# Optimization experiments

Hardware: AMD Instinct MI355X
Metric: run time of the kernel (lower is better)

The kernel has to match this reference:

```python
import jax, jax.numpy as jnp
import numpy as np

B, T, NF, D, H = 4, 32, 256, 512, 8
DK = D // H


def setup_inputs() -> dict:
    key = jax.random.key(0)
    ks = jax.random.split(key, 10)
    x = jax.random.normal(ks[0], (B, T, NF, D), dtype=jnp.float32)
    adj = jax.random.randint(ks[1], (NF, NF), 0, 2, dtype=jnp.int32)
    adj = adj.at[jnp.arange(NF), jnp.arange(NF)].set(1)  # self-loops avoid all-masked rows
    s = 1.0 / np.sqrt(D)
    Wq = jax.random.normal(ks[2], (D, D), dtype=jnp.float32) * s
    Wk = jax.random.normal(ks[3], (D, D), dtype=jnp.float32) * s
    Wv = jax.random.normal(ks[4], (D, D), dtype=jnp.float32) * s
    Wo = jax.random.normal(ks[5], (D, D), dtype=jnp.float32) * s
    bq = jnp.zeros((D,), jnp.float32)
    bk = jnp.zeros((D,), jnp.float32)
    bv = jnp.zeros((D,), jnp.float32)
    bo = jnp.zeros((D,), jnp.float32)
    return {"x": x, "adj": adj, "Wq": Wq, "bq": bq, "Wk": Wk, "bk": bk,
            "Wv": Wv, "bv": bv, "Wo": Wo, "bo": bo}


def reference(x, adj, Wq, bq, Wk, bk, Wv, bv, Wo, bo):
    b, t, nf, d = x.shape
    q = x @ Wq.T + bq
    k = x @ Wk.T + bk
    v = x @ Wv.T + bv
    # split heads: [B,T,Nf,H,dk]
    qh = q.reshape(b, t, nf, H, DK)
    kh = k.reshape(b, t, nf, H, DK)
    vh = v.reshape(b, t, nf, H, DK)
    scores = jnp.einsum('btihd,btjhd->bthij', qh, kh) / jnp.sqrt(jnp.float32(DK))
    mask = (adj > 0)  # [Nf,Nf], broadcast over b,t,h
    scores = jnp.where(mask[None, None, None], scores, jnp.float32(-jnp.inf))
    attn = jax.nn.softmax(scores, axis=-1)  # dropout is identity in eval
    out = jnp.einsum('bthij,btjhd->btihd', attn, vh).reshape(b, t, nf, d)
    return out @ Wo.T + bo
```

## Files before the change

kernel.cpp:

```cpp
#include <hip/hip_runtime.h>

#define NF 256
#define H_ 8
#define M_ 32768

typedef _Float16 f16;
typedef _Float16 f16x8 __attribute__((ext_vector_type(8)));
typedef float f32x4 __attribute__((ext_vector_type(4)));
typedef unsigned short u16x8 __attribute__((ext_vector_type(8)));
typedef unsigned int u32x2 __attribute__((ext_vector_type(2)));
typedef unsigned int u32x4 __attribute__((ext_vector_type(4)));

#define GLOAD16(src, dst) \
  __builtin_amdgcn_global_load_lds((const __attribute__((address_space(1))) void*)(src), \
                                   (__attribute__((address_space(3))) void*)(dst), 16, 0, 0)

#define LDS_FENCE() do { asm volatile("s_waitcnt lgkmcnt(0)" ::: "memory"); \
                         __builtin_amdgcn_sched_barrier(0); } while (0)
#define SBAR() asm volatile("s_barrier" ::: "memory")


__device__ __forceinline__ void stageHT(const f16* __restrict__ g, int r0, int k0,
                                        f16* ldst, int wave, int lane) {
    const int key = lane >> 3;
    const int colsw = k0 + (((lane & 7) ^ key) << 3);
#pragma unroll
    for (int i = 0; i < 2; ++i) {
        int r = i * 64 + wave * 8 + key;
        GLOAD16(g + (size_t)(r0 + r) * 512 + colsw, ldst + (i * 64 + wave * 8) * 64);
    }
}

__device__ __forceinline__ void gemm256_core(const f16* __restrict__ A, const f16* __restrict__ W,
                                             int m0, int n0, f16* lds,
                                             f32x4 (&acc)[8][4], int wave, int lane) {
    const int wr = wave & 1, wc = wave >> 1;
    const int l15 = lane & 15, l4 = lane >> 4;
    stageHT(W, n0,        0, lds + 16384, wave, lane);
    stageHT(W, n0 + 128,  0, lds + 24576, wave, lane);
    stageHT(A, m0,        0, lds,         wave, lane);
    stageHT(A, m0 + 128,  0, lds + 8192,  wave, lane);
    stageHT(W, n0,       64, lds + 32768 + 16384, wave, lane);
    stageHT(W, n0 + 128, 64, lds + 32768 + 24576, wave, lane);
    asm volatile("s_waitcnt vmcnt(4)" ::: "memory");
    SBAR();
#pragma unroll
    for (int t = 0; t < 8; ++t) {
        f16* bufA = lds + (t & 1) * 32768;
        f16* bufB = bufA + 16384;
        f16* nA   = lds + ((t & 1) ^ 1) * 32768;
        f16x8 bfr[4][2];
#pragma unroll
        for (int j = 0; j < 4; ++j)
#pragma unroll
            for (int kk = 0; kk < 2; ++kk) {
                int rb = wc * 64 + j * 16 + l15;
                bfr[j][kk] = *reinterpret_cast<const f16x8*>(
                    bufB + rb * 64 + ((((kk << 2) + l4) ^ (rb & 7)) << 3));
            }
#pragma unroll
        for (int q = 0; q < 4; ++q) {
            f16x8 afr[2][2];
#pragma unroll
            for (int rf = 0; rf < 2; ++rf)
#pragma unroll
                for (int kk = 0; kk < 2; ++kk) {
                    int ra = wr * 128 + q * 32 + rf * 16 + l15;
                    afr[rf][kk] = *reinterpret_cast<const f16x8*>(
                        bufA + ra * 64 + ((((kk << 2) + l4) ^ (ra & 7)) << 3));
                }
            if (q == 0 && t < 7) stageHT(A, m0,       (t + 1) * 64, nA,          wave, lane);
            if (q == 1 && t < 7) stageHT(A, m0 + 128, (t + 1) * 64, nA + 8192,   wave, lane);
            if (q == 2 && t < 6) stageHT(W, n0,       (t + 2) * 64, bufB,        wave, lane);
            if (q == 3 && t < 6) stageHT(W, n0 + 128, (t + 2) * 64, bufB + 8192, wave, lane);
            SBAR();
            LDS_FENCE();
            __builtin_amdgcn_s_setprio(1);
#pragma unroll
            for (int rf = 0; rf < 2; ++rf)
#pragma unroll
                for (int j = 0; j < 4; ++j)
#pragma unroll
                    for (int kk = 0; kk < 2; ++kk)
                        acc[q * 2 + rf][j] = __builtin_amdgcn_mfma_f32_16x16x32_f16(
                            afr[rf][kk], bfr[j][kk], acc[q * 2 + rf][j], 0, 0, 0);
            __builtin_amdgcn_s_setprio(0);
            if (q < 3) SBAR();
        }
        if (t < 6) { asm volatile("s_waitcnt vmcnt(4)" ::: "memory"); }
        else       { asm volatile("s_waitcnt vmcnt(0)" ::: "memory"); }
        SBAR();
    }
}


#define QSCALE 0.1803368801111204f

__global__ void prep_all(const float* __restrict__ x, f16* __restrict__ xh,
                         const float* __restrict__ Wq, const float* __restrict__ Wk,
                         const float* __restrict__ Wv, const float* __restrict__ Wo,
                         const float* __restrict__ bq, const float* __restrict__ bk,
                         const float* __restrict__ bv, const int* __restrict__ adj,
                         f16* __restrict__ Wh, f16* __restrict__ Woh,
                         float* __restrict__ biasAll, unsigned long long* __restrict__ bmask) {
    if (blockIdx.x < 2048) {
        int idx = blockIdx.x * 256 + threadIdx.x;
        for (; idx < M_ * 512 / 8; idx += 2048 * 256) {
            const float4* s = reinterpret_cast<const float4*>(x + (size_t)idx * 8);
            float4 v0 = s[0], v1 = s[1];
            f16x8 o;
            o[0] = (f16)v0.x; o[1] = (f16)v0.y; o[2] = (f16)v0.z; o[3] = (f16)v0.w;
            o[4] = (f16)v1.x; o[5] = (f16)v1.y; o[6] = (f16)v1.z; o[7] = (f16)v1.w;
            *reinterpret_cast<f16x8*>(xh + (size_t)idx * 8) = o;
        }
        return;
    }
    const int tid = (blockIdx.x - 2048) * 256 + threadIdx.x;
    {
        const float* s; f16* d; float sc = 1.0f;
        int pp = tid >> 15, off = tid & 32767;
        if (pp == 0)      { s = Wq; d = Wh;              sc = QSCALE; }
        else if (pp == 1) { s = Wk; d = Wh + 512 * 512; }
        else if (pp == 2) { s = Wv; d = Wh + 2 * 512 * 512; }
        else              { s = Wo; d = Woh; }
        const float4* sv4 = reinterpret_cast<const float4*>(s + (size_t)off * 8);
        float4 v0 = sv4[0], v1 = sv4[1];
        f16x8 o;
        o[0] = (f16)(v0.x * sc); o[1] = (f16)(v0.y * sc);
        o[2] = (f16)(v0.z * sc); o[3] = (f16)(v0.w * sc);
        o[4] = (f16)(v1.x * sc); o[5] = (f16)(v1.y * sc);
        o[6] = (f16)(v1.z * sc); o[7] = (f16)(v1.w * sc);
        *reinterpret_cast<f16x8*>(d + (size_t)off * 8) = o;
    }
    if (tid < 1536) {
        float v = (tid < 512) ? QSCALE * bq[tid] : (tid < 1024) ? bk[tid - 512] : bv[tid - 1024];
        biasAll[tid] = v;
    }
    if (tid < 65536) {
        unsigned long long bal = __ballot(adj[tid] > 0);
        if ((tid & 63) == 0) bmask[tid >> 6] = bal;
    }
}


__global__ __launch_bounds__(512) void qkv_gemm(const f16* __restrict__ A, const f16* __restrict__ W,
                                                const float* __restrict__ biasAll,
                                                f16* __restrict__ out, f16* __restrict__ vT) {
    __shared__ __align__(16) f16 lds[65536];
    const int tt = threadIdx.x, wave = tt >> 6, lane = tt & 63;
    const int lb = blockIdx.x, xcd = lb & 7, idx = lb >> 3;
    const int m0 = (xcd * 16 + idx / 6) * 256;
    const int n0 = (idx % 6) * 256;
    f32x4 acc[8][4] = {};
    gemm256_core(A, W, m0, n0, lds, acc, wave, lane);

    const int wr = wave & 1, wc = wave >> 1;
    const int l15 = lane & 15, l4 = lane >> 4;
    f16* epi = lds;
    const bool isV = (n0 >= 1024);
    float bb[4];
#pragma unroll
    for (int bc = 0; bc < 4; ++bc) bb[bc] = biasAll[n0 + wc * 64 + bc * 16 + l15];
#pragma unroll
    for (int half = 0; half < 2; ++half) {
        if (wr == half) {
            if (!isV) {
#pragma unroll
                for (int ar = 0; ar < 8; ++ar)
#pragma unroll
                    for (int bc = 0; bc < 4; ++bc)
#pragma unroll
                        for (int r = 0; r < 4; ++r)
                            epi[(ar * 16 + l4 * 4 + r) * 264 + wc * 64 + bc * 16 + l15] =
                                (f16)(acc[ar][bc][r] + bb[bc]);
            } else {
#pragma unroll
                for (int ar = 0; ar < 8; ++ar)
#pragma unroll
                    for (int bc = 0; bc < 4; ++bc)
#pragma unroll
                        for (int r = 0; r < 4; ++r)
                            epi[(wc * 64 + bc * 16 + l15) * 136 + ar * 16 + l4 * 4 + r] =
                                (f16)(acc[ar][bc][r] + bb[bc]);
            }
        }
        LDS_FENCE();
        SBAR();
        if (!isV) {
            const int rr = tt >> 5, slot = tt & 31;
#pragma unroll
            for (int p = 0; p < 8; ++p) {
                int row = p * 16 + rr;
                *reinterpret_cast<f16x8*>(out + (size_t)(m0 + half * 128 + row) * 1024 + n0 + slot * 8) =
                    *reinterpret_cast<const f16x8*>(epi + row * 264 + slot * 8);
            }
        } else {
            f16* vdst = vT + (size_t)(m0 >> 8) * 8 * 64 * 256 + (size_t)(n0 - 1024) * 256;
            const int dk = tt >> 1;
#pragma unroll
            for (int i = 0; i < 8; ++i) {
                int nf0 = (tt & 1) * 64 + i * 8;
                *reinterpret_cast<f16x8*>(vdst + (size_t)dk * 256 + half * 128 + nf0) =
                    *reinterpret_cast<const f16x8*>(epi + dk * 136 + nf0);
            }
        }
        SBAR();
    }
}


template <int NR>
__device__ __forceinline__ void stage_rows512(const f16* __restrict__ g, int ld, int coff,
                                              f16* ldsb, int wave, int lane) {
    const int rr = wave * 8 + (lane >> 3);
    const int p  = lane & 7;
#pragma unroll
    for (int i = 0; i < NR / 64; ++i) {
        int r = i * 64 + rr;
        int col = ((p ^ (r & 7)) << 3);
        GLOAD16(g + (size_t)r * ld + coff + col, ldsb + (i * 64 + wave * 8) * 64);
    }
}

__device__ __forceinline__ void stage_v512(const f16* __restrict__ g, f16* ldsb,
                                           int wave, int lane) {
    const int rr = wave * 8 + (lane >> 3);
    const int p  = lane & 7;
#pragma unroll
    for (int i = 0; i < 4; ++i) {
        int r = i * 64 + rr;
        int key = (r ^ (r >> 3)) & 7;
        GLOAD16(g + (size_t)r * 64 + ((p ^ key) << 3), ldsb + (i * 64 + wave * 8) * 64);
    }
}

__global__ __launch_bounds__(512, 2) void attn_kernel(const f16* __restrict__ qkv,
                                                      const f16* __restrict__ vT,
                                                      const unsigned long long* __restrict__ bmg,
                                                      f16* __restrict__ ao) {
    __shared__ f16 Ks[256 * 64];
    __shared__ f16 Vs[256 * 64];
    __shared__ unsigned long long BMs[1024];
    const int t = threadIdx.x, wave = t >> 6, lane = t & 63;
    const int l15 = lane & 15, l4 = lane >> 4;
    const int lb = blockIdx.x, xcd = lb & 7, idx = lb >> 3;
    const int bt = xcd * 16 + (idx >> 3), h = idx & 7;
    const int bh = bt * 8 + h;
    const int btq = bt * 256, hq = h * 64;
    const f16* qb = qkv + (size_t)btq * 1024 + hq;
    const f16* kb = qb + 512;

    stage_rows512<256>(kb, 1024, 0, Ks, wave, lane);
    stage_v512(vT + (size_t)bh * 16384, Vs, wave, lane);
    GLOAD16((const char*)bmg + (size_t)t * 16, (char*)(BMs + wave * 128));
    __syncthreads();

    for (int s = 0; s < 2; ++s) {
        const int qrow_base = wave * 32 + s * 16;

        f16x8 aq[2];
#pragma unroll
        for (int kk = 0; kk < 2; ++kk)
            aq[kk] = *reinterpret_cast<const f16x8*>(
                qb + (size_t)(qrow_base + l15) * 1024 + kk * 32 + l4 * 8);

        f32x4 sc[16];
#pragma unroll
        for (int ct = 0; ct < 16; ++ct) sc[ct] = (f32x4){0.f, 0.f, 0.f, 0.f};
        __builtin_amdgcn_s_setprio(1);
#pragma unroll
        for (int ct = 0; ct < 16; ++ct)
#pragma unroll
            for (int kk = 0; kk < 2; ++kk) {
                int rk = ct * 16 + l15;
                int sk = kk * 4 + l4;
                f16x8 bk_ = *reinterpret_cast<const f16x8*>(Ks + rk * 64 + ((sk ^ (rk & 7)) << 3));
                sc[ct] = __builtin_amdgcn_mfma_f32_16x16x32_f16(bk_, aq[kk], sc[ct], 0, 0, 0);
            }
        __builtin_amdgcn_s_setprio(0);

        float mx = -1e38f;
#pragma unroll
        for (int ct = 0; ct < 16; ++ct)
#pragma unroll
            for (int r = 0; r < 4; ++r) mx = fmaxf(mx, sc[ct][r]);
        mx = fmaxf(mx, __shfl_xor(mx, 16, 64));
        mx = fmaxf(mx, __shfl_xor(mx, 32, 64));

        const int ig = qrow_base + l15;
        const u16x8* mr = reinterpret_cast<const u16x8*>(BMs + ig * 4);
        u16x8 w0 = mr[0], w1 = mr[1];

        f32x4 oacc[4] = {};
        float sum = 0.f;
#pragma unroll
        for (int kkp = 0; kkp < 8; ++kkp) {
            const int ctA = 2 * kkp, ctB = 2 * kkp + 1;
            unsigned mbA = ((kkp < 4) ? (unsigned)w0[ctA] : (unsigned)w1[ctA & 7]) >> (l4 * 4);
            unsigned mbB = ((kkp < 4) ? (unsigned)w0[ctB] : (unsigned)w1[ctB & 7]) >> (l4 * 4);
            float pA0 = __builtin_exp2f(sc[ctA][0] - mx); pA0 = ((mbA >> 0) & 1u) ? pA0 : 0.0f;
            float pA1 = __builtin_exp2f(sc[ctA][1] - mx); pA1 = ((mbA >> 1) & 1u) ? pA1 : 0.0f;
            float pA2 = __builtin_exp2f(sc[ctA][2] - mx); pA2 = ((mbA >> 2) & 1u) ? pA2 : 0.0f;
            float pA3 = __builtin_exp2f(sc[ctA][3] - mx); pA3 = ((mbA >> 3) & 1u) ? pA3 : 0.0f;
            float pB0 = __builtin_exp2f(sc[ctB][0] - mx); pB0 = ((mbB >> 0) & 1u) ? pB0 : 0.0f;
            float pB1 = __builtin_exp2f(sc[ctB][1] - mx); pB1 = ((mbB >> 1) & 1u) ? pB1 : 0.0f;
            float pB2 = __builtin_exp2f(sc[ctB][2] - mx); pB2 = ((mbB >> 2) & 1u) ? pB2 : 0.0f;
            float pB3 = __builtin_exp2f(sc[ctB][3] - mx); pB3 = ((mbB >> 3) & 1u) ? pB3 : 0.0f;
            sum += (pA0 + pA1) + (pA2 + pA3) + (pB0 + pB1) + (pB2 + pB3);
            u32x4 up;
            up[0] = __builtin_bit_cast(unsigned int, __builtin_amdgcn_cvt_pkrtz(pA0, pA1));
            up[1] = __builtin_bit_cast(unsigned int, __builtin_amdgcn_cvt_pkrtz(pA2, pA3));
            up[2] = __builtin_bit_cast(unsigned int, __builtin_amdgcn_cvt_pkrtz(pB0, pB1));
            up[3] = __builtin_bit_cast(unsigned int, __builtin_amdgcn_cvt_pkrtz(pB2, pB3));
            f16x8 pa = __builtin_bit_cast(f16x8, up);
            __builtin_amdgcn_s_setprio(1);
#pragma unroll
            for (int c2 = 0; c2 < 4; ++c2) {
                int d = c2 * 16 + l15;
                int nf0a = kkp * 32 + l4 * 4;
                int nf0b = nf0a + 16;
                int rvA = d * 4 + (nf0a >> 6), rvB = d * 4 + (nf0b >> 6);
                int keyA = (rvA ^ (rvA >> 3)) & 7, keyB = (rvB ^ (rvB >> 3)) & 7;
                u32x2 va = *reinterpret_cast<const u32x2*>(
                    Vs + rvA * 64 + ((((nf0a >> 3) & 7) ^ keyA) << 3) + (nf0a & 7));
                u32x2 vb = *reinterpret_cast<const u32x2*>(
                    Vs + rvB * 64 + ((((nf0b >> 3) & 7) ^ keyB) << 3) + (nf0b & 7));
                u32x4 uv; uv[0] = va[0]; uv[1] = va[1]; uv[2] = vb[0]; uv[3] = vb[1];
                f16x8 bv_ = __builtin_bit_cast(f16x8, uv);
                oacc[c2] = __builtin_amdgcn_mfma_f32_16x16x32_f16(pa, bv_, oacc[c2], 0, 0, 0);
            }
            __builtin_amdgcn_s_setprio(0);
            __builtin_amdgcn_sched_barrier(0);
        }
        sum += __shfl_xor(sum, 16, 64);
        sum += __shfl_xor(sum, 32, 64);
        float rs = 1.0f / sum;
        float rsrow[4];
#pragma unroll
        for (int r = 0; r < 4; ++r) rsrow[r] = __shfl(rs, l4 * 4 + r, 64);

#pragma unroll
        for (int c2 = 0; c2 < 4; ++c2)
#pragma unroll
            for (int r = 0; r < 4; ++r) {
                int nf = qrow_base + l4 * 4 + r;
                int dcol = hq + c2 * 16 + l15;
                ao[((size_t)btq + nf) * 512 + dcol] = (f16)(oacc[c2][r] * rsrow[r]);
            }
    }
}


__global__ __launch_bounds__(512) void o_gemm(const f16* __restrict__ A, const f16* __restrict__ W,
                                              const float* __restrict__ bo, float* __restrict__ out) {
    __shared__ __align__(16) f16 lds[65536];
    const int tt = threadIdx.x, wave = tt >> 6, lane = tt & 63;
    const int lb = blockIdx.x, xcd = lb & 7, idx = lb >> 3;
    const int m0 = (xcd * 16 + idx / 2) * 256;
    const int n0 = (idx % 2) * 256;
    f32x4 acc[8][4] = {};
    gemm256_core(A, W, m0, n0, lds, acc, wave, lane);

    const int wr = wave & 1, wc = wave >> 1;
    const int l15 = lane & 15, l4 = lane >> 4;
    float bb[4];
#pragma unroll
    for (int bc = 0; bc < 4; ++bc) bb[bc] = bo[n0 + wc * 64 + bc * 16 + l15];
#pragma unroll
    for (int ar = 0; ar < 8; ++ar)
#pragma unroll
        for (int bc = 0; bc < 4; ++bc) {
            int ng = n0 + wc * 64 + bc * 16 + l15;
#pragma unroll
            for (int r = 0; r < 4; ++r) {
                int mg = m0 + wr * 128 + ar * 16 + l4 * 4 + r;
                out[(size_t)mg * 512 + ng] = acc[ar][bc][r] + bb[bc];
            }
        }
}


extern "C" void kernel_launch(void* const* d_in, const int* in_sizes, int n_in,
                              void* d_out, int out_size, void* d_ws, size_t ws_size,
                              hipStream_t stream) {
    const float* x   = (const float*)d_in[0];
    const int*   adj = (const int*)d_in[1];
    const float* Wq  = (const float*)d_in[2];
    const float* bq  = (const float*)d_in[3];
    const float* Wk  = (const float*)d_in[4];
    const float* bk  = (const float*)d_in[5];
    const float* Wv  = (const float*)d_in[6];
    const float* bv  = (const float*)d_in[7];
    const float* Wo  = (const float*)d_in[8];
    const float* bo  = (const float*)d_in[9];
    float* out = (float*)d_out;

    char* ws = (char*)d_ws;
    f16*   Wh      = (f16*)ws;
    f16*   Woh     = (f16*)(ws + 1572864);
    float* biasAll = (float*)(ws + 2097152);
    unsigned long long* bmask = (unsigned long long*)(ws + 2103296);
    f16*   xh      = (f16*)(ws + 2111488);
    f16*   qkvb    = (f16*)(ws + 2111488 + (size_t)M_ * 512 * 2);
    f16*   vTb     = (f16*)(ws + 2111488 + (size_t)M_ * 512 * 2 + (size_t)M_ * 1024 * 2);
    f16*   aob     = xh;

    prep_all<<<2560, 256, 0, stream>>>(x, xh, Wq, Wk, Wv, Wo, bq, bk, bv, adj,
                                       Wh, Woh, biasAll, bmask);
    qkv_gemm<<<768, 512, 0, stream>>>(xh, Wh, biasAll, qkvb, vTb);
    attn_kernel<<<128 * H_, 512, 0, stream>>>(qkvb, vTb, bmask, aob);
    o_gemm<<<256, 512, 0, stream>>>(aob, Woh, bo, out);
}
```

Before: 165.0 us.

## Fuse fp32-to-fp16 conversion of x into QKV GEMM A-tile loading

Removes the separate x conversion pass from the prep kernel and has the QKV GEMM load fp32 x directly into registers, convert it with packed round-toward-zero conversion, and write the f16 tile to LDS while prefetching the next k-step. This avoids writing and rereading a 32 MB fp16 copy of x. In exchange each GEMM tile reads fp32 data (twice the bytes) across the six column tiles, and uses more registers and manual LDS writes instead of asynchronous global-to-LDS loads. The rounding mode also changes from round-to-nearest to round-toward-zero.

```diff
diff --git a/kernel.cpp b/kernel.cpp
--- a/kernel.cpp
+++ b/kernel.cpp
@@ -19,6 +19,15 @@
                          __builtin_amdgcn_sched_barrier(0); } while (0)
 #define SBAR() asm volatile("s_barrier" ::: "memory")
 
+__device__ __forceinline__ f16x8 cvt8(float4 a, float4 b) {
+    u32x4 u;
+    u[0] = __builtin_bit_cast(unsigned int, __builtin_amdgcn_cvt_pkrtz(a.x, a.y));
+    u[1] = __builtin_bit_cast(unsigned int, __builtin_amdgcn_cvt_pkrtz(a.z, a.w));
+    u[2] = __builtin_bit_cast(unsigned int, __builtin_amdgcn_cvt_pkrtz(b.x, b.y));
+    u[3] = __builtin_bit_cast(unsigned int, __builtin_amdgcn_cvt_pkrtz(b.z, b.w));
+    return __builtin_bit_cast(f16x8, u);
+}
+
 
 __device__ __forceinline__ void stageHT(const f16* __restrict__ g, int r0, int k0,
                                         f16* ldst, int wave, int lane) {
@@ -30,6 +39,7 @@
         GLOAD16(g + (size_t)(r0 + r) * 512 + colsw, ldst + (i * 64 + wave * 8) * 64);
     }
 }
+
 
 __device__ __forceinline__ void gemm256_core(const f16* __restrict__ A, const f16* __restrict__ W,
                                              int m0, int n0, f16* lds,
@@ -96,26 +106,13 @@
 
 #define QSCALE 0.1803368801111204f
 
-__global__ void prep_all(const float* __restrict__ x, f16* __restrict__ xh,
-                         const float* __restrict__ Wq, const float* __restrict__ Wk,
+__global__ void prep_all(const float* __restrict__ Wq, const float* __restrict__ Wk,
                          const float* __restrict__ Wv, const float* __restrict__ Wo,
                          const float* __restrict__ bq, const float* __restrict__ bk,
                          const float* __restrict__ bv, const int* __restrict__ adj,
                          f16* __restrict__ Wh, f16* __restrict__ Woh,
                          float* __restrict__ biasAll, unsigned long long* __restrict__ bmask) {
-    if (blockIdx.x < 2048) {
-        int idx = blockIdx.x * 256 + threadIdx.x;
-        for (; idx < M_ * 512 / 8; idx += 2048 * 256) {
-            const float4* s = reinterpret_cast<const float4*>(x + (size_t)idx * 8);
-            float4 v0 = s[0], v1 = s[1];
-            f16x8 o;
-            o[0] = (f16)v0.x; o[1] = (f16)v0.y; o[2] = (f16)v0.z; o[3] = (f16)v0.w;
-            o[4] = (f16)v1.x; o[5] = (f16)v1.y; o[6] = (f16)v1.z; o[7] = (f16)v1.w;
-            *reinterpret_cast<f16x8*>(xh + (size_t)idx * 8) = o;
-        }
-        return;
-    }
-    const int tid = (blockIdx.x - 2048) * 256 + threadIdx.x;
+    const int tid = blockIdx.x * 256 + threadIdx.x;
     {
         const float* s; f16* d; float sc = 1.0f;
         int pp = tid >> 15, off = tid & 32767;
@@ -143,7 +140,7 @@
 }
 
 
-__global__ __launch_bounds__(512) void qkv_gemm(const f16* __restrict__ A, const f16* __restrict__ W,
+__global__ __launch_bounds__(512) void qkv_gemm(const float* __restrict__ x, const f16* __restrict__ W,
                                                 const float* __restrict__ biasAll,
                                                 f16* __restrict__ out, f16* __restrict__ vT) {
     __shared__ __align__(16) f16 lds[65536];
@@ -151,11 +148,114 @@
     const int lb = blockIdx.x, xcd = lb & 7, idx = lb >> 3;
     const int m0 = (xcd * 16 + idx / 6) * 256;
     const int n0 = (idx % 6) * 256;
-    f32x4 acc[8][4] = {};
-    gemm256_core(A, W, m0, n0, lds, acc, wave, lane);
-
     const int wr = wave & 1, wc = wave >> 1;
     const int l15 = lane & 15, l4 = lane >> 4;
+    const int key = lane >> 3, p = lane & 7;
+    const int colsw = ((p ^ key) << 3);
+    f32x4 acc[8][4] = {};
+    float4 lA[8];
+
+    stageHT(W, n0,        0, lds + 16384, wave, lane);
+    stageHT(W, n0 + 128,  0, lds + 24576, wave, lane);
+#pragma unroll
+    for (int half = 0; half < 2; ++half)
+#pragma unroll
+        for (int i = 0; i < 2; ++i) {
+            const float* src = x + (size_t)(m0 + half * 128 + i * 64 + wave * 8 + key) * 512 + colsw;
+            lA[half * 4 + i * 2]     = *reinterpret_cast<const float4*>(src);
+            lA[half * 4 + i * 2 + 1] = *reinterpret_cast<const float4*>(src + 4);
+        }
+    stageHT(W, n0,       64, lds + 32768 + 16384, wave, lane);
+    stageHT(W, n0 + 128, 64, lds + 32768 + 24576, wave, lane);
+#pragma unroll
+    for (int half = 0; half < 2; ++half)
+#pragma unroll
+        for (int i = 0; i < 2; ++i)
+            *reinterpret_cast<f16x8*>(lds + half * 8192 + (i * 64 + wave * 8 + key) * 64 + p * 8) =
+                cvt8(lA[half * 4 + i * 2], lA[half * 4 + i * 2 + 1]);
+    asm volatile("s_waitcnt vmcnt(4)" ::: "memory");
+    asm volatile("s_waitcnt lgkmcnt(0)" ::: "memory");
+    SBAR();
+
+#pragma unroll
+    for (int t = 0; t < 8; ++t) {
+        f16* bufA = lds + (t & 1) * 32768;
+        f16* bufB = bufA + 16384;
+        f16* nA   = lds + ((t & 1) ^ 1) * 32768;
+        f16x8 bfr[4][2];
+#pragma unroll
+        for (int j = 0; j < 4; ++j)
+#pragma unroll
+            for (int kk = 0; kk < 2; ++kk) {
+                int rb = wc * 64 + j * 16 + l15;
+                bfr[j][kk] = *reinterpret_cast<const f16x8*>(
+                    bufB + rb * 64 + ((((kk << 2) + l4) ^ (rb & 7)) << 3));
+            }
+#pragma unroll
+        for (int q = 0; q < 4; ++q) {
+            f16x8 afr[2][2];
+#pragma unroll
+            for (int rf = 0; rf < 2; ++rf)
+#pragma unroll
+                for (int kk = 0; kk < 2; ++kk) {
+                    int ra = wr * 128 + q * 32 + rf * 16 + l15;
+                    afr[rf][kk] = *reinterpret_cast<const f16x8*>(
+                        bufA + ra * 64 + ((((kk << 2) + l4) ^ (ra & 7)) << 3));
+                }
+            if (q == 0 && t < 7) {
+#pragma unroll
+                for (int i = 0; i < 2; ++i) {
+                    const float* src = x + (size_t)(m0 + i * 64 + wave * 8 + key) * 512 + (t + 1) * 64 + colsw;
+                    lA[i * 2]     = *reinterpret_cast<const float4*>(src);
+                    lA[i * 2 + 1] = *reinterpret_cast<const float4*>(src + 4);
+                }
+            }
+            if (q == 1 && t < 7) {
+#pragma unroll
+                for (int i = 0; i < 2; ++i) {
+                    const float* src = x + (size_t)(m0 + 128 + i * 64 + wave * 8 + key) * 512 + (t + 1) * 64 + colsw;
+                    lA[4 + i * 2]     = *reinterpret_cast<const float4*>(src);
+                    lA[4 + i * 2 + 1] = *reinterpret_cast<const float4*>(src + 4);
+                }
+            }
+            if (q == 2) {
+                if (t < 6) stageHT(W, n0, (t + 2) * 64, bufB, wave, lane);
+                if (t < 7) {
+#pragma unroll
+                    for (int i = 0; i < 2; ++i)
+                        *reinterpret_cast<f16x8*>(nA + (i * 64 + wave * 8 + key) * 64 + p * 8) =
+                            cvt8(lA[i * 2], lA[i * 2 + 1]);
+                }
+            }
+            if (q == 3) {
+                if (t < 6) stageHT(W, n0 + 128, (t + 2) * 64, bufB + 8192, wave, lane);
+                if (t < 7) {
+#pragma unroll
+                    for (int i = 0; i < 2; ++i)
+                        *reinterpret_cast<f16x8*>(nA + 8192 + (i * 64 + wave * 8 + key) * 64 + p * 8) =
+                            cvt8(lA[4 + i * 2], lA[4 + i * 2 + 1]);
+                }
+            }
+            SBAR();
+            LDS_FENCE();
+            __builtin_amdgcn_s_setprio(1);
+#pragma unroll
+            for (int rf = 0; rf < 2; ++rf)
+#pragma unroll
+                for (int j = 0; j < 4; ++j)
+#pragma unroll
+                    for (int kk = 0; kk < 2; ++kk)
+                        acc[q * 2 + rf][j] = __builtin_amdgcn_mfma_f32_16x16x32_f16(
+                            afr[rf][kk], bfr[j][kk], acc[q * 2 + rf][j], 0, 0, 0);
+            __builtin_amdgcn_s_setprio(0);
+            if (q < 3) SBAR();
+        }
+        if (t < 6) { asm volatile("s_waitcnt vmcnt(4)" ::: "memory"); }
+        else       { asm volatile("s_waitcnt vmcnt(0)" ::: "memory"); }
+        asm volatile("s_waitcnt lgkmcnt(0)" ::: "memory");
+        SBAR();
+    }
+
     f16* epi = lds;
     const bool isV = (n0 >= 1024);
     float bb[4];
@@ -189,8 +289,8 @@
         if (!isV) {
             const int rr = tt >> 5, slot = tt & 31;
 #pragma unroll
-            for (int p = 0; p < 8; ++p) {
-                int row = p * 16 + rr;
+            for (int pp2 = 0; pp2 < 8; ++pp2) {
+                int row = pp2 * 16 + rr;
                 *reinterpret_cast<f16x8*>(out + (size_t)(m0 + half * 128 + row) * 1024 + n0 + slot * 8) =
                     *reinterpret_cast<const f16x8*>(epi + row * 264 + slot * 8);
             }
@@ -400,14 +500,13 @@
     f16*   Woh     = (f16*)(ws + 1572864);
     float* biasAll = (float*)(ws + 2097152);
     unsigned long long* bmask = (unsigned long long*)(ws + 2103296);
-    f16*   xh      = (f16*)(ws + 2111488);
+    f16*   aob     = (f16*)(ws + 2111488);
     f16*   qkvb    = (f16*)(ws + 2111488 + (size_t)M_ * 512 * 2);
     f16*   vTb     = (f16*)(ws + 2111488 + (size_t)M_ * 512 * 2 + (size_t)M_ * 1024 * 2);
-    f16*   aob     = xh;
-
-    prep_all<<<2560, 256, 0, stream>>>(x, xh, Wq, Wk, Wv, Wo, bq, bk, bv, adj,
-                                       Wh, Woh, biasAll, bmask);
-    qkv_gemm<<<768, 512, 0, stream>>>(xh, Wh, biasAll, qkvb, vTb);
+
+    prep_all<<<512, 256, 0, stream>>>(Wq, Wk, Wv, Wo, bq, bk, bv, adj,
+                                      Wh, Woh, biasAll, bmask);
+    qkv_gemm<<<768, 512, 0, stream>>>(x, Wh, biasAll, qkvb, vTb);
     attn_kernel<<<128 * H_, 512, 0, stream>>>(qkvb, vTb, bmask, aob);
     o_gemm<<<256, 512, 0, stream>>>(aob, Woh, bo, out);
 }
```

Result: slower. 199.0 us (+20.6%).
